# Kernel optimization log

Measured on AMD Instinct MI355X. Metric: run time of the kernel, lower is better.

## Reference

```python
import jax, jax.numpy as jnp
import numpy as np

HEADS = 16
D_MODEL = 1024
D_K = D_MODEL // HEADS
B, S = 2, 2048
NEG = -1000000000.0


def setup_inputs() -> dict:
    key = jax.random.key(0)
    ks = jax.random.split(key, 8)
    q = jax.random.normal(ks[0], (B, S, D_MODEL), dtype=jnp.float32)
    k = jax.random.normal(ks[1], (B, S, D_MODEL), dtype=jnp.float32)
    v = jax.random.normal(ks[2], (B, S, D_MODEL), dtype=jnp.float32)
    mask = jax.random.randint(ks[3], (B, 1, S, S), 0, 2) > 0  # True = masked
    scale = 1.0 / np.sqrt(D_MODEL)
    Wq = jax.random.normal(ks[4], (D_MODEL, D_MODEL), dtype=jnp.float32) * scale
    Wk = jax.random.normal(ks[5], (D_MODEL, D_MODEL), dtype=jnp.float32) * scale
    Wv = jax.random.normal(ks[6], (D_MODEL, D_MODEL), dtype=jnp.float32) * scale
    Wo = jax.random.normal(ks[7], (D_MODEL, D_MODEL), dtype=jnp.float32) * scale
    return {"q": q, "k": k, "v": v, "mask": mask,
            "Wq": Wq, "Wk": Wk, "Wv": Wv, "Wo": Wo}


def reference(q, k, v, mask, Wq, Wk, Wv, Wo):
    b, s, _ = q.shape
    # torch Linear: x @ W.T ; reshape to [B, H, S, d_k]
    def proj(x, W):
        return (x @ W.T).reshape(b, -1, HEADS, D_K).transpose(0, 2, 1, 3)
    qh, kh, vh = proj(q, Wq), proj(k, Wk), proj(v, Wv)
    # scaled dot-product attention; scale uses d_k (key.shape[-1] after reshape)
    att = jnp.einsum('bhqd,bhkd->bhqk', qh, kh) / jnp.sqrt(jnp.float32(D_K))
    att = jnp.where(mask, NEG, att)
    att = jax.nn.softmax(att, axis=-1)
    out = jnp.einsum('bhqk,bhkd->bhqd', att, vh)  # [B,H,S,d_k]
    out = out.transpose(0, 2, 1, 3).reshape(b, -1, D_MODEL)
    return out @ Wo.T  # dropout is identity at inference
```

## Files before the change

### kernel.cpp

```cpp
#include <hip/hip_runtime.h>

typedef unsigned short u16;
typedef unsigned int   u32;
typedef unsigned char  u8;
typedef unsigned long long u64;
typedef __attribute__((ext_vector_type(8))) short bf16x8;
typedef __attribute__((ext_vector_type(4))) float f32x4;
typedef __attribute__((ext_vector_type(16))) float f32x16;

__device__ __forceinline__ u16 f2b(float f) {
  union { float f; u32 u; } v; v.f = f;
  u32 u = v.u;
  return (u16)((u + 0x7fffu + ((u >> 16) & 1u)) >> 16);
}
__device__ __forceinline__ float b2f(u16 x) {
  union { u32 u; float f; } v; v.u = ((u32)x) << 16; return v.f;
}
__device__ __forceinline__ u32 pk2(u16 lo, u16 hi) { return (u32)lo | ((u32)hi << 16); }

__device__ __forceinline__ float fexp2(float x) { return __builtin_amdgcn_exp2f(x); }

__device__ __forceinline__ u32 cvtpk(float lo, float hi) {
  u32 r;
  asm("v_cvt_pk_bf16_f32 %0, %1, %2" : "=v"(r) : "v"(lo), "v"(hi));
  return r;
}

__device__ __forceinline__ void swap32(u32& a, u32& b) {
  asm("v_permlane32_swap_b32 %0, %1" : "+v"(a), "+v"(b));
}

__device__ __forceinline__ void glds16(const u16* g, u16* l) {
  __builtin_amdgcn_global_load_lds((const __attribute__((address_space(1))) void*)g,
                                   (__attribute__((address_space(3))) void*)l, 16, 0, 0);
}

__global__ __launch_bounds__(256) void mask_detect(const u8* __restrict__ raw,
                                                   int* __restrict__ flag) {
  int i = blockIdx.x * 256 + threadIdx.x;
  uint4 x = ((const uint4*)raw)[i];
  u32 o = x.x | x.y | x.z | x.w;
  u64 b1 = __ballot((o & 0x0000ff00u) != 0);
  u64 b2 = __ballot((o & 0xffff0000u) != 0);
  if ((threadIdx.x & 63) == 0) {
    if (b1) atomicOr(&flag[0], 1);
    if (b2) atomicOr(&flag[1], 1);
  }
}

__global__ __launch_bounds__(256) void mask_bits(const u8* __restrict__ raw,
                                                 u64* __restrict__ out,
                                                 const int* __restrict__ flag) {
  int f = flag[0] ? 2 : (flag[1] ? 1 : 0);
  int i = blockIdx.x * 256 + threadIdx.x;
  bool bit;
  if (f == 2)      bit = raw[i] != 0;
  else if (f == 0) bit = ((const int*)raw)[i] != 0;
  else             bit = ((const float*)raw)[i] != 0.0f;
  u64 b = __ballot(bit);
  if ((threadIdx.x & 63) == 0) out[i >> 6] = b;
}

__global__ __launch_bounds__(256) void conv_all(
    const float* __restrict__ W0, const float* __restrict__ W1,
    const float* __restrict__ W2, const float* __restrict__ W3,
    const float* __restrict__ A0, const float* __restrict__ A1,
    const float* __restrict__ A2,
    u16* __restrict__ o0, u16* __restrict__ o1, u16* __restrict__ o2,
    u16* __restrict__ o3, u16* __restrict__ o4, u16* __restrict__ o5,
    u16* __restrict__ o6) {
  int gid = blockIdx.x * 256 + threadIdx.x;
  const float* src; u16* dst; int off;
  if (gid < 524288) {
    int wz = gid >> 17; off = (gid & 131071) * 8;
    src = wz == 0 ? W0 : wz == 1 ? W1 : wz == 2 ? W2 : W3;
    dst = wz == 0 ? o0 : wz == 1 ? o1 : wz == 2 ? o2 : o3;
  } else {
    int g2 = gid - 524288;
    int az = g2 >> 19; off = (g2 & 524287) * 8;
    src = az == 0 ? A0 : az == 1 ? A1 : A2;
    dst = az == 0 ? o4 : az == 1 ? o5 : o6;
  }
  float4 a = *(const float4*)(src + off), b2 = *(const float4*)(src + off + 4);
  uint4 t;
  t.x = pk2(f2b(a.x), f2b(a.y));   t.y = pk2(f2b(a.z), f2b(a.w));
  t.z = pk2(f2b(b2.x), f2b(b2.y)); t.w = pk2(f2b(b2.z), f2b(b2.w));
  *(uint4*)(dst + off) = t;
}

template<int CF32>
__device__ __forceinline__ void gemm_body(
    const u16* __restrict__ Av, const u16* __restrict__ Bv, void* __restrict__ Cv,
    int N, int K, int m0, int n0, float cscale, u16* As, u16* Bs) {
  const int tid = threadIdx.x;
  const int lane = tid & 63, w = tid >> 6;
  const int lr = lane & 15, lg = lane >> 4;
  const int wm = (w >> 1) * 64, wn = (w & 1) * 64;
  const int srow = lane >> 3;
  const int selem = (((lane & 7) ^ srow) << 3);
  const int rsw = (lr & 7) << 3;

  f32x4 acc[4][4];
#pragma unroll
  for (int mi = 0; mi < 4; ++mi)
#pragma unroll
    for (int ni = 0; ni < 4; ++ni)
      acc[mi][ni] = (f32x4){0.f, 0.f, 0.f, 0.f};

#define GSTAGE(buf, k0_)                                                       \
  do {                                                                         \
    _Pragma("unroll")                                                          \
    for (int r_ = 0; r_ < 4; ++r_) {                                           \
      const int c_ = w * 4 + r_;                                               \
      const int row_ = c_ * 8 + srow;                                          \
      glds16(Av + (size_t)(m0 + row_) * K + (k0_) + selem, As + (buf) * 8192 + c_ * 512); \
      glds16(Bv + (size_t)(n0 + row_) * K + (k0_) + selem, Bs + (buf) * 8192 + c_ * 512); \
    }                                                                          \
  } while (0)

  GSTAGE(0, 0);
  __syncthreads();
  int cur = 0;
  for (int k0 = 0; k0 < K; k0 += 64) {
    if (k0 + 64 < K) GSTAGE(cur ^ 1, k0 + 64);
    bf16x8 af[4][2], bfv[4][2];
#pragma unroll
    for (int mi = 0; mi < 4; ++mi)
#pragma unroll
      for (int kk = 0; kk < 2; ++kk)
        af[mi][kk] = *(bf16x8*)&As[cur * 8192 + (wm + mi * 16 + lr) * 64 + ((kk * 32 + lg * 8) ^ rsw)];
#pragma unroll
    for (int ni = 0; ni < 4; ++ni)
#pragma unroll
      for (int kk = 0; kk < 2; ++kk)
        bfv[ni][kk] = *(bf16x8*)&Bs[cur * 8192 + (wn + ni * 16 + lr) * 64 + ((kk * 32 + lg * 8) ^ rsw)];
    __builtin_amdgcn_s_setprio(1);
#pragma unroll
    for (int mi = 0; mi < 4; ++mi)
#pragma unroll
      for (int ni = 0; ni < 4; ++ni)
#pragma unroll
        for (int kk = 0; kk < 2; ++kk)
          acc[mi][ni] = __builtin_amdgcn_mfma_f32_16x16x32_bf16(
              af[mi][kk], bfv[ni][kk], acc[mi][ni], 0, 0, 0);
    __builtin_amdgcn_s_setprio(0);
    __syncthreads();
    cur ^= 1;
  }
#undef GSTAGE
#pragma unroll
  for (int mi = 0; mi < 4; ++mi)
#pragma unroll
    for (int ni = 0; ni < 4; ++ni)
#pragma unroll
      for (int r = 0; r < 4; ++r) {
        int m = m0 + wm + mi * 16 + lg * 4 + r;
        int n = n0 + wn + ni * 16 + lr;
        float vv = acc[mi][ni][r] * cscale;
        if (CF32) ((float*)Cv)[(size_t)m * N + n] = vv;
        else      ((u16*)Cv)[(size_t)m * N + n] = f2b(vv);
      }
}

__global__ __launch_bounds__(256) void gemm_qkv(
    const u16* __restrict__ qb, const u16* __restrict__ kb, const u16* __restrict__ vb,
    const u16* __restrict__ Wqb, const u16* __restrict__ Wkb, const u16* __restrict__ Wvb,
    u16* __restrict__ Qb, u16* __restrict__ Kb, u16* __restrict__ VTb, float qscale) {
  __shared__ __align__(16) u16 As[2 * 8192];
  __shared__ __align__(16) u16 Bs[2 * 8192];
  const int z = blockIdx.z;
  const u16 *Av, *Bv; u16* Cv; int N, bxx, by; float cs = 1.0f;
  if (z < 2) {
    Av = z ? kb : qb; Bv = z ? Wkb : Wqb; Cv = z ? Kb : Qb;
    N = 1024; bxx = blockIdx.x & 7; by = blockIdx.x >> 3;
    if (!z) cs = qscale;
  } else {
    Av = Wvb; Bv = vb; Cv = VTb;
    N = 4096; bxx = blockIdx.x & 31; by = blockIdx.x >> 5;
  }
  gemm_body<0>(Av, Bv, Cv, N, 1024, by * 128, bxx * 128, cs, As, Bs);
}

__global__ __launch_bounds__(256) void gemm_o(
    const u16* __restrict__ Ob, const u16* __restrict__ Wob, float* __restrict__ C) {
  __shared__ __align__(16) u16 As[2 * 8192];
  __shared__ __align__(16) u16 Bs[2 * 8192];
  gemm_body<1>(Ob, Wob, C, 1024, 1024, blockIdx.y * 128, blockIdx.x * 128, 1.0f, As, Bs);
}

__global__ __launch_bounds__(256, 4) void flash12(const u16* __restrict__ Q,
                                                  const u16* __restrict__ K,
                                                  const u16* __restrict__ VT,
                                                  const u64* __restrict__ mpk,
                                                  u16* __restrict__ O0,
                                                  u16* __restrict__ O1,
                                                  u16* __restrict__ O2,
                                                  float* __restrict__ Lp) {
  __shared__ __align__(16) u16 Ks[2][4096];
  __shared__ __align__(16) u16 Vs[2][4096];
  const int tid = threadIdx.x, lane = tid & 63, w = tid >> 6;
  const int c = lane & 31, h = lane >> 5;
  const int bid = blockIdx.x;
  const int xcd = bid & 7, idx = bid >> 3;
  const int gl = idx >> 4, qblk = idx & 15;
  const int group = xcd * 12 + gl;
  const int split = group % 3;
  const int hb = group / 3;
  const int head = hb & 15, b = hb >> 4;
  const int qw = qblk * 128 + w * 32;
  const int kt0 = (split * 32) / 3;
  const int ktn = ((split + 1) * 32) / 3;
  const int nt = ktn - kt0;
  const size_t kbase = (size_t)b * 2048 * 1024 + (size_t)head * 64;
  const size_t vbase = (size_t)head * 64 * 4096 + (size_t)b * 2048;
  const int srow = lane >> 3;
  const int selem = (((lane & 7) ^ srow) << 3);
  const int rswc = (c & 7) << 3;

  bf16x8 qf[4];
#pragma unroll
  for (int kd = 0; kd < 4; ++kd)
    qf[kd] = *(const bf16x8*)&Q[kbase + (size_t)(qw + c) * 1024 + 16 * kd + 8 * h];

  union { u32 u[4]; bf16x8 v; } ones;
#pragma unroll
  for (int i = 0; i < 4; ++i) ones.u[i] = 0x3f803f80u;

  f32x16 accO0, accO1, accL;
#pragma unroll
  for (int i = 0; i < 16; ++i) { accO0[i] = 0.f; accO1[i] = 0.f; accL[i] = 0.f; }

  const u64* mrp = mpk + ((size_t)b * 2048 + qw + c) * 32;

#define STAGE(buf, t)                                                          \
  do {                                                                         \
    const int k0_ = (t) * 64;                                                  \
    _Pragma("unroll")                                                          \
    for (int r_ = 0; r_ < 2; ++r_) {                                           \
      const int c_ = w * 2 + r_;                                               \
      const int row_ = c_ * 8 + srow;                                          \
      glds16(K + kbase + (size_t)(k0_ + row_) * 1024 + selem, &Ks[buf][c_ * 512]); \
    }                                                                          \
    _Pragma("unroll")                                                          \
    for (int r_ = 0; r_ < 2; ++r_) {                                           \
      const int c_ = w * 2 + r_;                                               \
      const int row_ = c_ * 8 + srow;                                          \
      glds16(VT + vbase + (size_t)row_ * 4096 + k0_ + selem, &Vs[buf][c_ * 512]); \
    }                                                                          \
  } while (0)

  STAGE(0, kt0);
  u64 mb_next = mrp[kt0];
  __syncthreads();

  int cur = 0;
  for (int t = 0; t < nt; ++t) {
    const u64 mb = mb_next;
    if (t + 1 < nt) {
      STAGE(cur ^ 1, kt0 + t + 1);
      mb_next = mrp[kt0 + t + 1];
    }
    const u16* ks = Ks[cur];
    const u16* vs = Vs[cur];
    f32x16 s0, s1;
#pragma unroll
    for (int i = 0; i < 16; ++i) { s0[i] = 0.f; s1[i] = 0.f; }
    __builtin_amdgcn_s_setprio(1);
#pragma unroll
    for (int kd = 0; kd < 4; ++kd) {
      bf16x8 kf0 = *(bf16x8*)&ks[c * 64 + ((16 * kd + 8 * h) ^ rswc)];
      s0 = __builtin_amdgcn_mfma_f32_32x32x16_bf16(kf0, qf[kd], s0, 0, 0, 0);
      bf16x8 kf1 = *(bf16x8*)&ks[(32 + c) * 64 + ((16 * kd + 8 * h) ^ rswc)];
      s1 = __builtin_amdgcn_mfma_f32_32x32x16_bf16(kf1, qf[kd], s1, 0, 0, 0);
    }
    __builtin_amdgcn_s_setprio(0);
    u32 pw[2][4][2];
#pragma unroll
    for (int kb = 0; kb < 2; ++kb) {
      const u32 m32 = (u32)(mb >> (32 * kb + 4 * h));
      float pp[16];
#pragma unroll
      for (int g = 0; g < 4; ++g)
#pragma unroll
        for (int r = 0; r < 4; ++r) {
          float e = fexp2(kb == 0 ? s0[4 * g + r] : s1[4 * g + r]);
          pp[4 * g + r] = ((m32 >> (8 * g + r)) & 1) ? 0.0f : e;
        }
#pragma unroll
      for (int g = 0; g < 4; ++g)
#pragma unroll
        for (int hh = 0; hh < 2; ++hh)
          pw[kb][g][hh] = cvtpk(pp[4 * g + 2 * hh], pp[4 * g + 2 * hh + 1]);
    }
    __builtin_amdgcn_s_setprio(1);
#pragma unroll
    for (int kb = 0; kb < 2; ++kb)
#pragma unroll
      for (int s = 0; s < 2; ++s) {
        u32 w0 = pw[kb][2 * s][0], w2 = pw[kb][2 * s + 1][0];
        swap32(w0, w2);
        u32 w1 = pw[kb][2 * s][1], w3 = pw[kb][2 * s + 1][1];
        swap32(w1, w3);
        union { u32 u[4]; bf16x8 v; } af;
        af.u[0] = w0; af.u[1] = w1; af.u[2] = w2; af.u[3] = w3;
        const int ksg = kb * 2 + s;
        bf16x8 vf0 = *(bf16x8*)&vs[c * 64 + ((16 * ksg + 8 * h) ^ rswc)];
        accO0 = __builtin_amdgcn_mfma_f32_32x32x16_bf16(af.v, vf0, accO0, 0, 0, 0);
        bf16x8 vf1 = *(bf16x8*)&vs[(32 + c) * 64 + ((16 * ksg + 8 * h) ^ rswc)];
        accO1 = __builtin_amdgcn_mfma_f32_32x32x16_bf16(af.v, vf1, accO1, 0, 0, 0);
        accL  = __builtin_amdgcn_mfma_f32_32x32x16_bf16(af.v, ones.v, accL, 0, 0, 0);
      }
    __builtin_amdgcn_s_setprio(0);
    __syncthreads();
    cur ^= 1;
  }
#undef STAGE
  u16* Op = split == 0 ? O0 : split == 1 ? O1 : O2;
  const size_t obase = (size_t)b * 2048 + qw;
#pragma unroll
  for (int g = 0; g < 4; ++g)
#pragma unroll
    for (int r = 0; r < 4; ++r) {
      const int qrow = r + 8 * g + 4 * h;
      const size_t row = obase + qrow;
      const size_t base = row * 1024 + (size_t)head * 64 + c;
      Op[base]      = f2b(accO0[4 * g + r]);
      Op[base + 32] = f2b(accO1[4 * g + r]);
      if (c == 0) Lp[(size_t)split * 65536 + row * 16 + head] = accL[4 * g + r];
    }
}

__global__ __launch_bounds__(256) void combine(const u16* __restrict__ O0,
                                               const u16* __restrict__ O1,
                                               const u16* __restrict__ O2,
                                               const float* __restrict__ Lp,
                                               u16* __restrict__ Ob) {
  int gid = blockIdx.x * 256 + threadIdx.x;
  int row = gid >> 7, chb = (gid & 127) * 8;
  int head = chb >> 6;
  float l = Lp[(size_t)row * 16 + head] + Lp[65536 + (size_t)row * 16 + head] +
            Lp[131072 + (size_t)row * 16 + head];
  float inv = 1.0f / l;
  size_t off = (size_t)row * 1024 + chb;
  union { uint4 q; u16 s[8]; } a, b, c2, o;
  a.q  = *(const uint4*)(O0 + off);
  b.q  = *(const uint4*)(O1 + off);
  c2.q = *(const uint4*)(O2 + off);
#pragma unroll
  for (int j = 0; j < 8; ++j)
    o.s[j] = f2b((b2f(a.s[j]) + b2f(b.s[j]) + b2f(c2.s[j])) * inv);
  *(uint4*)(Ob + off) = o.q;
}

extern "C" void kernel_launch(void* const* d_in, const int* in_sizes, int n_in,
                              void* d_out, int out_size, void* d_ws, size_t ws_size,
                              hipStream_t stream) {
  const float* q    = (const float*)d_in[0];
  const float* k    = (const float*)d_in[1];
  const float* v    = (const float*)d_in[2];
  const u8*    mask = (const u8*)d_in[3];
  const float* Wq   = (const float*)d_in[4];
  const float* Wk   = (const float*)d_in[5];
  const float* Wv   = (const float*)d_in[6];
  const float* Wo   = (const float*)d_in[7];

  u8* ws = (u8*)d_ws;
  int* flag = (int*)ws;
  u64* mpk  = (u64*)(ws + 256);
  u16* Wqb  = (u16*)(ws + 256 + (1u << 20));
  u16* Wkb  = Wqb + (1 << 20);
  u16* Wvb  = Wkb + (1 << 20);
  u16* Wob  = Wvb + (1 << 20);
  const size_t NE = (size_t)4096 * 1024;
  u16* vb   = Wob + (1 << 20);
  u16* O2   = vb;
  u16* Qb   = vb + NE;
  u16* Kb   = Qb + NE;
  u16* VTb  = Kb + NE;
  u16* qb   = (u16*)d_out;
  u16* kb   = qb + NE;
  u16* O0   = qb;
  u16* O1   = kb;
  float* Lp = (float*)Wqb;
  u16* Ob   = Qb;

  const float LOG2E = 1.4426950408889634f;

  hipMemsetAsync(flag, 0, 8, stream);
  mask_detect<<<32, 256, 0, stream>>>(mask, flag);
  mask_bits<<<32768, 256, 0, stream>>>(mask, mpk, flag);
  conv_all<<<8192, 256, 0, stream>>>(Wq, Wk, Wv, Wo, q, k, v,
                                     Wqb, Wkb, Wvb, Wob, qb, kb, vb);

  gemm_qkv<<<dim3(256, 1, 3), 256, 0, stream>>>(
      qb, kb, vb, Wqb, Wkb, Wvb, Qb, Kb, VTb, 0.125f * LOG2E);

  flash12<<<1536, 256, 0, stream>>>(Qb, Kb, VTb, mpk, O0, O1, O2, Lp);
  combine<<<2048, 256, 0, stream>>>(O0, O1, O2, Lp, Ob);

  gemm_o<<<dim3(8, 32), 256, 0, stream>>>(Ob, Wob, (float*)d_out);
}
```

Baseline: 162.9 us.

## Fuse fp32-to-bf16 activation conversion into QKV GEMM loads; remap gemm_o blocks per XCD

The fp32 activations q, k, v are no longer converted to bf16 by a separate pass. The QKV GEMM now loads fp32 tiles into registers, converts them with v_cvt_pk_bf16_f32, and writes them swizzled into LDS, double-buffered across the k-loop. This removes a full write and reread of the bf16 activation copies. In exchange it reads twice as many bytes per element inside the GEMM and raises register pressure. The output GEMM also switches to a 1D grid so that nearby M blocks land on the same XCD, for better L2 reuse.

Result: slower. 170.3 us (+4.6%).

```diff
diff --git a/kernel.cpp b/kernel.cpp
--- a/kernel.cpp
+++ b/kernel.cpp
@@ -61,36 +61,24 @@
   if ((threadIdx.x & 63) == 0) out[i >> 6] = b;
 }
 
-__global__ __launch_bounds__(256) void conv_all(
-    const float* __restrict__ W0, const float* __restrict__ W1,
-    const float* __restrict__ W2, const float* __restrict__ W3,
-    const float* __restrict__ A0, const float* __restrict__ A1,
-    const float* __restrict__ A2,
-    u16* __restrict__ o0, u16* __restrict__ o1, u16* __restrict__ o2,
-    u16* __restrict__ o3, u16* __restrict__ o4, u16* __restrict__ o5,
-    u16* __restrict__ o6) {
-  int gid = blockIdx.x * 256 + threadIdx.x;
-  const float* src; u16* dst; int off;
-  if (gid < 524288) {
-    int wz = gid >> 17; off = (gid & 131071) * 8;
-    src = wz == 0 ? W0 : wz == 1 ? W1 : wz == 2 ? W2 : W3;
-    dst = wz == 0 ? o0 : wz == 1 ? o1 : wz == 2 ? o2 : o3;
-  } else {
-    int g2 = gid - 524288;
-    int az = g2 >> 19; off = (g2 & 524287) * 8;
-    src = az == 0 ? A0 : az == 1 ? A1 : A2;
-    dst = az == 0 ? o4 : az == 1 ? o5 : o6;
-  }
-  float4 a = *(const float4*)(src + off), b2 = *(const float4*)(src + off + 4);
+__global__ __launch_bounds__(256) void conv_w(const float* __restrict__ W0, const float* __restrict__ W1,
+                                              const float* __restrict__ W2, const float* __restrict__ W3,
+                                              u16* __restrict__ o0, u16* __restrict__ o1,
+                                              u16* __restrict__ o2, u16* __restrict__ o3) {
+  int zz = blockIdx.z;
+  const float* W = zz == 0 ? W0 : zz == 1 ? W1 : zz == 2 ? W2 : W3;
+  u16* o = zz == 0 ? o0 : zz == 1 ? o1 : zz == 2 ? o2 : o3;
+  int i = (blockIdx.x * 256 + threadIdx.x) * 8;
+  float4 a = *(const float4*)(W + i), b2 = *(const float4*)(W + i + 4);
   uint4 t;
   t.x = pk2(f2b(a.x), f2b(a.y));   t.y = pk2(f2b(a.z), f2b(a.w));
   t.z = pk2(f2b(b2.x), f2b(b2.y)); t.w = pk2(f2b(b2.z), f2b(b2.w));
-  *(uint4*)(dst + off) = t;
-}
-
-template<int CF32>
+  *(uint4*)(o + i) = t;
+}
+
+template<int AF32, int BF32, int CF32>
 __device__ __forceinline__ void gemm_body(
-    const u16* __restrict__ Av, const u16* __restrict__ Bv, void* __restrict__ Cv,
+    const void* __restrict__ Av, const void* __restrict__ Bv, void* __restrict__ Cv,
     int N, int K, int m0, int n0, float cscale, u16* As, u16* Bs) {
   const int tid = threadIdx.x;
   const int lane = tid & 63, w = tid >> 6;
@@ -107,22 +95,58 @@
     for (int ni = 0; ni < 4; ++ni)
       acc[mi][ni] = (f32x4){0.f, 0.f, 0.f, 0.f};
 
-#define GSTAGE(buf, k0_)                                                       \
+  float4 fa0[4], fa1[4], fb0[4], fb1[4];
+
+#define GLDS_SIDE(P, base, k0_, LB)                                            \
   do {                                                                         \
     _Pragma("unroll")                                                          \
     for (int r_ = 0; r_ < 4; ++r_) {                                           \
       const int c_ = w * 4 + r_;                                               \
       const int row_ = c_ * 8 + srow;                                          \
-      glds16(Av + (size_t)(m0 + row_) * K + (k0_) + selem, As + (buf) * 8192 + c_ * 512); \
-      glds16(Bv + (size_t)(n0 + row_) * K + (k0_) + selem, Bs + (buf) * 8192 + c_ * 512); \
+      glds16((const u16*)(P) + (size_t)((base) + row_) * K + (k0_) + selem, (LB) + c_ * 512); \
     }                                                                          \
   } while (0)
 
-  GSTAGE(0, 0);
+#define F32_ISSUE(P, base, k0_, f0, f1)                                        \
+  do {                                                                         \
+    _Pragma("unroll")                                                          \
+    for (int rr = 0; rr < 4; ++rr) {                                           \
+      const int ch_ = rr * 256 + tid;                                          \
+      const int row_ = ch_ >> 3, col_ = (ch_ & 7) * 8;                         \
+      const float* p_ = (const float*)(P) + (size_t)((base) + row_) * K + (k0_) + col_; \
+      f0[rr] = *(const float4*)p_;                                             \
+      f1[rr] = *(const float4*)(p_ + 4);                                       \
+    }                                                                          \
+  } while (0)
+
+#define F32_WRITE(LB, f0, f1)                                                  \
+  do {                                                                         \
+    _Pragma("unroll")                                                          \
+    for (int rr = 0; rr < 4; ++rr) {                                           \
+      const int ch_ = rr * 256 + tid;                                          \
+      const int row_ = ch_ >> 3, col_ = (ch_ & 7) * 8;                         \
+      uint4 t_;                                                                \
+      t_.x = cvtpk(f0[rr].x, f0[rr].y); t_.y = cvtpk(f0[rr].z, f0[rr].w);      \
+      t_.z = cvtpk(f1[rr].x, f1[rr].y); t_.w = cvtpk(f1[rr].z, f1[rr].w);      \
+      *(uint4*)&(LB)[row_ * 64 + (col_ ^ ((row_ & 7) << 3))] = t_;             \
+    }                                                                          \
+  } while (0)
+
+  if (AF32) { F32_ISSUE(Av, m0, 0, fa0, fa1); F32_WRITE(As, fa0, fa1); }
+  else      GLDS_SIDE(Av, m0, 0, As);
+  if (BF32) { F32_ISSUE(Bv, n0, 0, fb0, fb1); F32_WRITE(Bs, fb0, fb1); }
+  else      GLDS_SIDE(Bv, n0, 0, Bs);
   __syncthreads();
+
   int cur = 0;
   for (int k0 = 0; k0 < K; k0 += 64) {
-    if (k0 + 64 < K) GSTAGE(cur ^ 1, k0 + 64);
+    const bool nx = (k0 + 64 < K);
+    if (nx) {
+      if (AF32) F32_ISSUE(Av, m0, k0 + 64, fa0, fa1);
+      else      GLDS_SIDE(Av, m0, k0 + 64, As + (cur ^ 1) * 8192);
+      if (BF32) F32_ISSUE(Bv, n0, k0 + 64, fb0, fb1);
+      else      GLDS_SIDE(Bv, n0, k0 + 64, Bs + (cur ^ 1) * 8192);
+    }
     bf16x8 af[4][2], bfv[4][2];
 #pragma unroll
     for (int mi = 0; mi < 4; ++mi)
@@ -144,10 +168,16 @@
           acc[mi][ni] = __builtin_amdgcn_mfma_f32_16x16x32_bf16(
               af[mi][kk], bfv[ni][kk], acc[mi][ni], 0, 0, 0);
     __builtin_amdgcn_s_setprio(0);
+    if (nx) {
+      if (AF32) F32_WRITE(As + (cur ^ 1) * 8192, fa0, fa1);
+      if (BF32) F32_WRITE(Bs + (cur ^ 1) * 8192, fb0, fb1);
+    }
     __syncthreads();
     cur ^= 1;
   }
-#undef GSTAGE
+#undef GLDS_SIDE
+#undef F32_ISSUE
+#undef F32_WRITE
 #pragma unroll
   for (int mi = 0; mi < 4; ++mi)
 #pragma unroll
@@ -163,29 +193,33 @@
 }
 
 __global__ __launch_bounds__(256) void gemm_qkv(
-    const u16* __restrict__ qb, const u16* __restrict__ kb, const u16* __restrict__ vb,
+    const float* __restrict__ q, const float* __restrict__ k, const float* __restrict__ v,
     const u16* __restrict__ Wqb, const u16* __restrict__ Wkb, const u16* __restrict__ Wvb,
     u16* __restrict__ Qb, u16* __restrict__ Kb, u16* __restrict__ VTb, float qscale) {
   __shared__ __align__(16) u16 As[2 * 8192];
   __shared__ __align__(16) u16 Bs[2 * 8192];
   const int z = blockIdx.z;
-  const u16 *Av, *Bv; u16* Cv; int N, bxx, by; float cs = 1.0f;
   if (z < 2) {
-    Av = z ? kb : qb; Bv = z ? Wkb : Wqb; Cv = z ? Kb : Qb;
-    N = 1024; bxx = blockIdx.x & 7; by = blockIdx.x >> 3;
-    if (!z) cs = qscale;
+    const float* act = z ? k : q;
+    const u16* Wb = z ? Wkb : Wqb;
+    u16* Cb = z ? Kb : Qb;
+    const int bxx = blockIdx.x & 7, by = blockIdx.x >> 3;
+    gemm_body<1, 0, 0>(act, Wb, Cb, 1024, 1024, by * 128, bxx * 128,
+                       z ? 1.0f : qscale, As, Bs);
   } else {
-    Av = Wvb; Bv = vb; Cv = VTb;
-    N = 4096; bxx = blockIdx.x & 31; by = blockIdx.x >> 5;
+    const int bxx = blockIdx.x & 31, by = blockIdx.x >> 5;
+    gemm_body<0, 1, 0>(Wvb, v, VTb, 4096, 1024, by * 128, bxx * 128, 1.0f, As, Bs);
   }
-  gemm_body<0>(Av, Bv, Cv, N, 1024, by * 128, bxx * 128, cs, As, Bs);
 }
 
 __global__ __launch_bounds__(256) void gemm_o(
     const u16* __restrict__ Ob, const u16* __restrict__ Wob, float* __restrict__ C) {
   __shared__ __align__(16) u16 As[2 * 8192];
   __shared__ __align__(16) u16 Bs[2 * 8192];
-  gemm_body<1>(Ob, Wob, C, 1024, 1024, blockIdx.y * 128, blockIdx.x * 128, 1.0f, As, Bs);
+  const int idx = blockIdx.x;
+  const int xcd = idx & 7, r = idx >> 3;
+  const int mblk = xcd * 4 + (r & 3), nblk = r >> 2;
+  gemm_body<0, 0, 1>(Ob, Wob, C, 1024, 1024, mblk * 128, nblk * 128, 1.0f, As, Bs);
 }
 
 __global__ __launch_bounds__(256, 4) void flash12(const u16* __restrict__ Q,
@@ -372,15 +406,12 @@
   u16* Wvb  = Wkb + (1 << 20);
   u16* Wob  = Wvb + (1 << 20);
   const size_t NE = (size_t)4096 * 1024;
-  u16* vb   = Wob + (1 << 20);
-  u16* O2   = vb;
-  u16* Qb   = vb + NE;
+  u16* O2   = Wob + (1 << 20);
+  u16* Qb   = O2 + NE;
   u16* Kb   = Qb + NE;
   u16* VTb  = Kb + NE;
-  u16* qb   = (u16*)d_out;
-  u16* kb   = qb + NE;
-  u16* O0   = qb;
-  u16* O1   = kb;
+  u16* O0   = (u16*)d_out;
+  u16* O1   = O0 + NE;
   float* Lp = (float*)Wqb;
   u16* Ob   = Qb;
 
@@ -389,14 +420,13 @@
   hipMemsetAsync(flag, 0, 8, stream);
   mask_detect<<<32, 256, 0, stream>>>(mask, flag);
   mask_bits<<<32768, 256, 0, stream>>>(mask, mpk, flag);
-  conv_all<<<8192, 256, 0, stream>>>(Wq, Wk, Wv, Wo, q, k, v,
-                                     Wqb, Wkb, Wvb, Wob, qb, kb, vb);
+  conv_w<<<dim3(512, 1, 4), 256, 0, stream>>>(Wq, Wk, Wv, Wo, Wqb, Wkb, Wvb, Wob);
 
   gemm_qkv<<<dim3(256, 1, 3), 256, 0, stream>>>(
-      qb, kb, vb, Wqb, Wkb, Wvb, Qb, Kb, VTb, 0.125f * LOG2E);
+      q, k, v, Wqb, Wkb, Wvb, Qb, Kb, VTb, 0.125f * LOG2E);
 
   flash12<<<1536, 256, 0, stream>>>(Qb, Kb, VTb, mpk, O0, O1, O2, Lp);
   combine<<<2048, 256, 0, stream>>>(O0, O1, O2, Lp, Ob);
 
-  gemm_o<<<dim3(8, 32), 256, 0, stream>>>(Ob, Wob, (float*)d_out);
-}
+  gemm_o<<<dim3(256), 256, 0, stream>>>(Ob, Wob, (float*)d_out);
+}
```
